# Kernel tuning notes

Hardware: AMD Instinct MI355X
Metric: run time of the kernel (lower is better)

Reference implementation:

```python
import jax, jax.numpy as jnp
import numpy as np

EMBED_DIM = 1024
HEAD = 16
DK = EMBED_DIM // HEAD  # 64
B, S = 2, 2048
NEG = -1.0e9


def setup_inputs() -> dict:
    key = jax.random.key(0)
    ks = jax.random.split(key, 8)
    d = {
        'query': jax.random.normal(ks[0], (B, S, EMBED_DIM), jnp.float32),
        'key': jax.random.normal(ks[1], (B, S, EMBED_DIM), jnp.float32),
        'value': jax.random.normal(ks[2], (B, S, EMBED_DIM), jnp.float32),
        'masked': jax.random.randint(ks[3], (B, S, S), 0, 2).astype(bool),
        'Wq': jax.random.normal(ks[4], (EMBED_DIM, EMBED_DIM), jnp.float32) / np.sqrt(EMBED_DIM),
        'Wk': jax.random.normal(ks[5], (EMBED_DIM, EMBED_DIM), jnp.float32) / np.sqrt(EMBED_DIM),
        'Wv': jax.random.normal(ks[6], (EMBED_DIM, EMBED_DIM), jnp.float32) / np.sqrt(EMBED_DIM),
        'Wo': jax.random.normal(ks[7], (EMBED_DIM, EMBED_DIM), jnp.float32) / np.sqrt(EMBED_DIM),
    }
    return d


def reference(query, key, value, masked, Wq, Wk, Wv, Wo):
    # projections (bias-free Linear: x @ W), split into heads: [B, H, S, DK]
    def split_heads(x):
        b, s, _ = x.shape
        return x.reshape(b, s, HEAD, DK).transpose(0, 2, 1, 3)

    q = split_heads(query @ Wq)
    k = split_heads(key @ Wk)
    v = split_heads(value @ Wv)

    scale = 1.0 / jnp.sqrt(jnp.asarray(DK, q.dtype))
    scores = jnp.einsum('bhqd,bhkd->bhqk', q, k) * scale
    scores = jnp.where(masked[:, None, :, :], NEG, scores)
    attn = jax.nn.softmax(scores, axis=-1)
    out = jnp.einsum('bhqk,bhkd->bhqd', attn, v)  # [B, H, S, DK]
    out = out.transpose(0, 2, 1, 3).reshape(query.shape[0], -1, EMBED_DIM)
    return out @ Wo
```

## Files before the change

### kernel.cpp

```cpp
#include <hip/hip_runtime.h>
#include <hip/hip_bf16.h>

typedef float f32x4 __attribute__((ext_vector_type(4)));
typedef __bf16 bf16x8 __attribute__((ext_vector_type(8)));
typedef _Float16 f16x2 __attribute__((ext_vector_type(2)));
typedef _Float16 f16x4 __attribute__((ext_vector_type(4)));

__device__ __forceinline__ unsigned short f2bf(float f){
  unsigned int u = __builtin_bit_cast(unsigned int, f);
  u += 0x7fffu + ((u >> 16) & 1u);
  return (unsigned short)(u >> 16);
}
__device__ __forceinline__ float bf2f(unsigned short h){
  return __builtin_bit_cast(float, (unsigned int)h << 16);
}

__device__ __forceinline__ f16x2 pkrtz(float a, float b){
  return __builtin_bit_cast(f16x2, __builtin_amdgcn_cvt_pkrtz(a, b));
}

__device__ __forceinline__ void glds16(const void* g, void* l){
  __builtin_amdgcn_global_load_lds((const __attribute__((address_space(1))) void*)g,
                                   (__attribute__((address_space(3))) void*)l, 16, 0, 0);
}

__device__ __forceinline__ f32x4 mfma16(bf16x8 a, bf16x8 b, f32x4 c){
  return __builtin_amdgcn_mfma_f32_16x16x32_bf16(a, b, c, 0, 0, 0);
}
__device__ __forceinline__ f32x4 mfma16h(f16x4 a, f16x4 b, f32x4 c){
  return __builtin_amdgcn_mfma_f32_16x16x16f16(a, b, c, 0, 0, 0);
}

#if __has_builtin(__builtin_amdgcn_exp2f)
__device__ __forceinline__ float exp2v(float x){ return __builtin_amdgcn_exp2f(x); }
#else
__device__ __forceinline__ float exp2v(float x){ return exp2f(x); }
#endif

__global__ void pack_mask_kernel(const unsigned char* __restrict__ m8,
                                 unsigned int* __restrict__ mp){
  const int wid = threadIdx.x >> 6, lane = threadIdx.x & 63;
  const int row = blockIdx.x * 4 + wid;
  const unsigned int* w32 = (const unsigned int*)m8;
  int bad = 0;
  #pragma unroll
  for(int c = 0; c < 1024; c += 64) bad |= (w32[c + lane] > 1u);
  const int is32 = !__any(bad);
  const int* m32 = (const int*)m8;
  for(int c0 = 0; c0 < 2048; c0 += 64){
    int mv = is32 ? m32[(size_t)row*2048 + c0 + lane]
                  : (int)m8[(size_t)row*2048 + c0 + lane];
    unsigned long long b = __ballot(mv != 0);
    if(lane == 0){
      mp[(size_t)row*64 + (c0 >> 5)]     = (unsigned int)b;
      mp[(size_t)row*64 + (c0 >> 5) + 1] = (unsigned int)(b >> 32);
    }
  }
}

__global__ void cvt3_kernel(const float* __restrict__ qs, const float* __restrict__ ks,
                            const float* __restrict__ vs, unsigned short* __restrict__ dst){
  const float* src = (blockIdx.y==0)?qs:(blockIdx.y==1)?ks:vs;
  unsigned short* d = dst + (size_t)blockIdx.y * 4194304;
  int i = blockIdx.x * 256 + threadIdx.x;
  const float4* s = (const float4*)src;
  float4 a = s[2*i], b = s[2*i+1];
  union { unsigned short h[8]; uint4 v; } o;
  o.h[0]=f2bf(a.x); o.h[1]=f2bf(a.y); o.h[2]=f2bf(a.z); o.h[3]=f2bf(a.w);
  o.h[4]=f2bf(b.x); o.h[5]=f2bf(b.y); o.h[6]=f2bf(b.z); o.h[7]=f2bf(b.w);
  ((uint4*)d)[i] = o.v;
}

__global__ void transW_kernel(const float* __restrict__ Wq, const float* __restrict__ Wk,
                              const float* __restrict__ Wv, const float* __restrict__ Wo,
                              unsigned short* __restrict__ WT){
  const float* W = (blockIdx.y==0)?Wq:(blockIdx.y==1)?Wk:(blockIdx.y==2)?Wv:Wo;
  const float scale = (blockIdx.y==0) ? 0.1803368801111601f : 1.0f;
  unsigned short* D = WT + (size_t)blockIdx.y * 1048576;
  int r0 = (blockIdx.x >> 4) * 64, c0 = (blockIdx.x & 15) * 64;
  __shared__ unsigned short T[64][65];
  int t = threadIdx.x;
  {
    int r = t >> 2, cb = (t & 3) * 16;
    const float4* src = (const float4*)(W + (size_t)(r0 + r) * 1024 + (c0 + cb));
    float4 v0 = src[0], v1 = src[1], v2 = src[2], v3 = src[3];
    float vals[16] = {v0.x,v0.y,v0.z,v0.w, v1.x,v1.y,v1.z,v1.w,
                      v2.x,v2.y,v2.z,v2.w, v3.x,v3.y,v3.z,v3.w};
    #pragma unroll
    for(int j=0;j<16;j++) T[cb + j][r] = f2bf(vals[j] * scale);
  }
  __syncthreads();
  {
    int c = t >> 2, rb = (t & 3) * 16;
    union { unsigned short h[16]; uint4 v[2]; } o;
    #pragma unroll
    for(int j=0;j<16;j++) o.h[j] = T[c][rb + j];
    uint4* dp = (uint4*)(D + (size_t)(c0 + c) * 1024 + (r0 + rb));
    dp[0] = o.v[0]; dp[1] = o.v[1];
  }
}

template<int OUTF32>
__global__ __launch_bounds__(256,2) void gemm_bt(
    const unsigned short* __restrict__ A0, const unsigned short* __restrict__ A1, const unsigned short* __restrict__ A2,
    const unsigned short* __restrict__ B0, const unsigned short* __restrict__ B1, const unsigned short* __restrict__ B2,
    unsigned short* __restrict__ C0, unsigned short* __restrict__ C1, unsigned short* __restrict__ C2,
    float* __restrict__ Cf)
{
  const unsigned short* A  = (blockIdx.z==0)?A0:(blockIdx.z==1)?A1:A2;
  const unsigned short* BT = (blockIdx.z==0)?B0:(blockIdx.z==1)?B1:B2;
  unsigned short* C        = (blockIdx.z==0)?C0:(blockIdx.z==1)?C1:C2;
  __shared__ unsigned short Asm[2][128*64];
  __shared__ unsigned short Bsm[2][128*64];
  const int wid = threadIdx.x >> 6, lane = threadIdx.x & 63;
  const int m0 = blockIdx.x * 128, n0 = blockIdx.y * 128;
  const int wrow = wid >> 1, wcol = wid & 1;
  const int li = lane & 15, lg = lane >> 4, li7 = lane & 7;
  f32x4 acc[4][4] = {};
  const int sr = lane >> 3;
  const int sc = lane & 7;
  const int sblk = sc ^ sr;

  #pragma unroll
  for(int i=0;i<4;i++){
    int r = wid*32 + i*8 + sr;
    glds16(A  + (size_t)(m0 + r)*1024 + sblk*8, &Asm[0][(wid*32 + i*8)*64]);
    glds16(BT + (size_t)(n0 + r)*1024 + sblk*8, &Bsm[0][(wid*32 + i*8)*64]);
  }
  __syncthreads();

  int buf = 0;
  for(int kt = 0; kt < 16; ++kt){
    if(kt < 15){
      const int kofs = (kt + 1) * 64;
      #pragma unroll
      for(int i=0;i<4;i++){
        int r = wid*32 + i*8 + sr;
        glds16(A  + (size_t)(m0 + r)*1024 + kofs + sblk*8, &Asm[buf^1][(wid*32 + i*8)*64]);
        glds16(BT + (size_t)(n0 + r)*1024 + kofs + sblk*8, &Bsm[buf^1][(wid*32 + i*8)*64]);
      }
    }
    #pragma unroll
    for(int kk=0; kk<2; kk++){
      bf16x8 af[4], bfv[4];
      #pragma unroll
      for(int fm=0; fm<4; fm++){
        int row = wrow*64 + fm*16 + li;
        int blk = (kk*4 + lg) ^ li7;
        af[fm] = *(const bf16x8*)&Asm[buf][row*64 + blk*8];
      }
      #pragma unroll
      for(int fn=0; fn<4; fn++){
        int row = wcol*64 + fn*16 + li;
        int blk = (kk*4 + lg) ^ li7;
        bfv[fn] = *(const bf16x8*)&Bsm[buf][row*64 + blk*8];
      }
      __builtin_amdgcn_s_setprio(1);
      #pragma unroll
      for(int fm=0; fm<4; fm++)
        #pragma unroll
        for(int fn=0; fn<4; fn++)
          acc[fm][fn] = mfma16(af[fm], bfv[fn], acc[fm][fn]);
      __builtin_amdgcn_s_setprio(0);
    }
    __syncthreads();
    buf ^= 1;
  }
  if(OUTF32 == 0 && blockIdx.z == 2){
    #pragma unroll
    for(int fm=0; fm<4; fm++){
      #pragma unroll
      for(int fn=0; fn<4; fn++){
        int col  = n0 + wcol*64 + fn*16 + li;
        int rowb = m0 + wrow*64 + fm*16 + lg*4;
        int bq = rowb >> 11, s = rowb & 2047;
        union { f16x2 h2[2]; unsigned long long u; } o;
        o.h2[0] = pkrtz(acc[fm][fn][0], acc[fm][fn][1]);
        o.h2[1] = pkrtz(acc[fm][fn][2], acc[fm][fn][3]);
        *(unsigned long long*)&C[((size_t)(bq*16 + (col>>6))*64 + (col&63))*2048 + s] = o.u;
      }
    }
  } else {
    #pragma unroll
    for(int fm=0; fm<4; fm++){
      #pragma unroll
      for(int fn=0; fn<4; fn++){
        int col  = n0 + wcol*64 + fn*16 + li;
        int rowb = m0 + wrow*64 + fm*16 + lg*4;
        #pragma unroll
        for(int r=0;r<4;r++){
          if(OUTF32) Cf[(size_t)(rowb + r)*1024 + col] = acc[fm][fn][r];
          else       C [(size_t)(rowb + r)*1024 + col] = f2bf(acc[fm][fn][r]);
        }
      }
    }
  }
}

__global__ __launch_bounds__(256,2) void attn_kernel(
    const unsigned short* __restrict__ Q, const unsigned short* __restrict__ K,
    const unsigned short* __restrict__ Vt, unsigned short* __restrict__ O,
    const unsigned int* __restrict__ mp)
{
  __shared__ unsigned short Ksm[2][64*64];
  __shared__ unsigned short Vsm[2][64*64];
  const int wid = threadIdx.x >> 6, lane = threadIdx.x & 63;
  const int orig = blockIdx.x;
  const int wg = (orig & 7) * 64 + (orig >> 3);
  const int qt = wg & 15, bh = wg >> 4;
  const int b = bh >> 4, h = bh & 15;
  const int q0 = qt * 128;
  const int li = lane & 15, lg = lane >> 4;
  const int li7 = li & 7;

  const int rowA = b*2048 + q0 + wid*32 + li;
  const int rowB = rowA + 16;

  bf16x8 qfA[2], qfB[2];
  {
    const unsigned short* qa = Q + (size_t)rowA*1024 + h*64 + lg*8;
    const unsigned short* qb = Q + (size_t)rowB*1024 + h*64 + lg*8;
    qfA[0] = *(const bf16x8*)qa; qfA[1] = *(const bf16x8*)(qa + 32);
    qfB[0] = *(const bf16x8*)qb; qfB[1] = *(const bf16x8*)(qb + 32);
  }

  f32x4 oaccA[4] = {}, oaccB[4] = {};
  float lrowA = 0.f, lrowB = 0.f;

  const int srow = lane >> 3;
  const int sblk = (lane & 7) ^ srow;

  #pragma unroll
  for(int i=0;i<2;i++){
    int r = wid*16 + i*8 + srow;
    glds16(K  + (size_t)(b*2048 + r)*1024 + h*64 + sblk*8, &Ksm[0][(wid*16 + i*8)*64]);
    glds16(Vt + (size_t)(bh*64 + r)*2048 + sblk*8,         &Vsm[0][(wid*16 + i*8)*64]);
  }
  uint2 mwA = *(const uint2*)&mp[(size_t)rowA*64];
  uint2 mwB = *(const uint2*)&mp[(size_t)rowB*64];
  uint2 mwAn, mwBn;
  __syncthreads();

  int buf = 0;
  for(int t = 0; t < 32; ++t){
    const int kv0 = t * 64;
    if(t < 31){
      #pragma unroll
      for(int i=0;i<2;i++){
        int r = wid*16 + i*8 + srow;
        glds16(K  + (size_t)(b*2048 + kv0 + 64 + r)*1024 + h*64 + sblk*8, &Ksm[buf^1][(wid*16 + i*8)*64]);
        glds16(Vt + (size_t)(bh*64 + r)*2048 + kv0 + 64 + sblk*8,         &Vsm[buf^1][(wid*16 + i*8)*64]);
      }
      mwAn = *(const uint2*)&mp[(size_t)rowA*64 + (size_t)((kv0 + 64) >> 5)];
      mwBn = *(const uint2*)&mp[(size_t)rowB*64 + (size_t)((kv0 + 64) >> 5)];
    }
    f32x4 pA[4], pB[4];
    __builtin_amdgcn_s_setprio(1);
    #pragma unroll
    for(int f=0; f<4; f++){
      f32x4 sa = {0.f,0.f,0.f,0.f}, sb = {0.f,0.f,0.f,0.f};
      #pragma unroll
      for(int kf=0; kf<2; kf++){
        int blk = (kf*4 + lg) ^ li7;
        bf16x8 kfr = *(const bf16x8*)&Ksm[buf][(f*16 + li)*64 + blk*8];
        sa = mfma16(kfr, qfA[kf], sa);
        sb = mfma16(kfr, qfB[kf], sb);
      }
      pA[f] = sa; pB[f] = sb;
    }
    __builtin_amdgcn_s_setprio(0);
    #pragma unroll
    for(int f=0; f<4; f++){
      unsigned int wA = (f < 2) ? mwA.x : mwA.y;
      unsigned int wB = (f < 2) ? mwB.x : mwB.y;
      float eA[4], eB[4];
      #pragma unroll
      for(int j=0;j<4;j++){
        unsigned int bitA = (wA >> ((f & 1)*16 + lg*4 + j)) & 1u;
        unsigned int bitB = (wB >> ((f & 1)*16 + lg*4 + j)) & 1u;
        float vA = exp2v(pA[f][j]);
        float vB = exp2v(pB[f][j]);
        eA[j] = bitA ? 0.f : vA;
        eB[j] = bitB ? 0.f : vB;
      }
      lrowA += (eA[0] + eA[1]) + (eA[2] + eA[3]);
      lrowB += (eB[0] + eB[1]) + (eB[2] + eB[3]);
      union { f16x2 h2[2]; f16x4 v; } ua, ub;
      ua.h2[0] = pkrtz(eA[0], eA[1]);
      ua.h2[1] = pkrtz(eA[2], eA[3]);
      ub.h2[0] = pkrtz(eB[0], eB[1]);
      ub.h2[1] = pkrtz(eB[2], eB[3]);
      const int blk = (f*2 + (lg >> 1)) ^ li7;
      const int sub = (lg & 1)*4;
      __builtin_amdgcn_s_setprio(1);
      #pragma unroll
      for(int dt=0; dt<4; dt++){
        f16x4 vf = *(const f16x4*)&Vsm[buf][(dt*16 + li)*64 + blk*8 + sub];
        oaccA[dt] = mfma16h(ua.v, vf, oaccA[dt]);
        oaccB[dt] = mfma16h(ub.v, vf, oaccB[dt]);
      }
      __builtin_amdgcn_s_setprio(0);
    }
    __syncthreads();
    mwA = mwAn; mwB = mwBn;
    buf ^= 1;
  }
  float rsA = lrowA, rsB = lrowB;
  rsA += __shfl_xor(rsA, 16); rsA += __shfl_xor(rsA, 32);
  rsB += __shfl_xor(rsB, 16); rsB += __shfl_xor(rsB, 32);
  float invA = 1.0f / rsA;
  float invB = 1.0f / rsB;
  #pragma unroll
  for(int r=0;r<4;r++){
    float ioA = __shfl(invA, lg*4 + r);
    float ioB = __shfl(invB, lg*4 + r);
    size_t rbA = (size_t)(b*2048 + q0 + wid*32 + lg*4 + r);
    size_t rbB = rbA + 16;
    #pragma unroll
    for(int dt=0; dt<4; dt++){
      O[rbA*1024 + h*64 + 16*dt + li] = f2bf(oaccA[dt][r] * ioA);
      O[rbB*1024 + h*64 + 16*dt + li] = f2bf(oaccB[dt][r] * ioB);
    }
  }
}

extern "C" void kernel_launch(void* const* d_in, const int* in_sizes, int n_in,
                              void* d_out, int out_size, void* d_ws, size_t ws_size,
                              hipStream_t stream)
{
  const float* q_in = (const float*)d_in[0];
  const float* k_in = (const float*)d_in[1];
  const float* v_in = (const float*)d_in[2];
  const unsigned char* mask = (const unsigned char*)d_in[3];
  const float* Wq = (const float*)d_in[4];
  const float* Wk = (const float*)d_in[5];
  const float* Wv = (const float*)d_in[6];
  const float* Wo = (const float*)d_in[7];

  char* ws = (char*)d_ws;
  const size_t MB = 1024*1024;
  unsigned short* XQ = (unsigned short*)(ws + 256);
  unsigned short* XK = (unsigned short*)(ws + 256 + 8*MB);
  unsigned short* XV = (unsigned short*)(ws + 256 + 16*MB);
  unsigned short* WT = (unsigned short*)(ws + 256 + 24*MB);
  unsigned short* Qb = (unsigned short*)(ws + 256 + 32*MB);
  unsigned short* Kb = (unsigned short*)(ws + 256 + 40*MB);
  unsigned short* Vt = (unsigned short*)(ws + 256 + 48*MB);
  unsigned short* Ob = XQ;
  unsigned int*   mpk= (unsigned int*)XV;

  cvt3_kernel<<<dim3(2048,3), 256, 0, stream>>>(q_in, k_in, v_in, XQ);
  transW_kernel<<<dim3(256,4), 256, 0, stream>>>(Wq, Wk, Wv, Wo, WT);
  gemm_bt<0><<<dim3(32,8,3), 256, 0, stream>>>(XQ, XK, XV,
                                               WT, WT + 1048576, WT + 2097152,
                                               Qb, Kb, Vt, nullptr);
  pack_mask_kernel<<<1024, 256, 0, stream>>>(mask, mpk);
  attn_kernel<<<512, 256, 0, stream>>>(Qb, Kb, Vt, Ob, mpk);
  gemm_bt<1><<<dim3(32,8,1), 256, 0, stream>>>(Ob, Ob, Ob,
                                               WT + 3*1048576, WT + 3*1048576, WT + 3*1048576,
                                               nullptr, nullptr, nullptr, (float*)d_out);
}
```

Measured before the change: 151.1 us.

## Double KV tile to 128 in attention and single-buffer projection GEMM

The attention kernel now stages 128 keys/values per iteration, with a 16-wide XOR swizzle for the V tile and 128-bit mask loads, which halves the number of loop iterations and barriers. The projection GEMM drops its double-buffered LDS prefetch in favour of a single buffer loaded and synced every k-step. That lowers LDS use but exposes global load latency, since loads no longer overlap compute. The larger attention tile raises LDS per block, which may limit occupancy.

Measured after the change: 145.5 us. 1.04x faster.

```diff
diff --git a/kernel.cpp b/kernel.cpp
--- a/kernel.cpp
+++ b/kernel.cpp
@@ -110,8 +110,8 @@
   const unsigned short* A  = (blockIdx.z==0)?A0:(blockIdx.z==1)?A1:A2;
   const unsigned short* BT = (blockIdx.z==0)?B0:(blockIdx.z==1)?B1:B2;
   unsigned short* C        = (blockIdx.z==0)?C0:(blockIdx.z==1)?C1:C2;
-  __shared__ unsigned short Asm[2][128*64];
-  __shared__ unsigned short Bsm[2][128*64];
+  __shared__ unsigned short Asm[128*64];
+  __shared__ unsigned short Bsm[128*64];
   const int wid = threadIdx.x >> 6, lane = threadIdx.x & 63;
   const int m0 = blockIdx.x * 128, n0 = blockIdx.y * 128;
   const int wrow = wid >> 1, wcol = wid & 1;
@@ -119,27 +119,17 @@
   f32x4 acc[4][4] = {};
   const int sr = lane >> 3;
   const int sc = lane & 7;
-  const int sblk = sc ^ sr;
-
-  #pragma unroll
-  for(int i=0;i<4;i++){
-    int r = wid*32 + i*8 + sr;
-    glds16(A  + (size_t)(m0 + r)*1024 + sblk*8, &Asm[0][(wid*32 + i*8)*64]);
-    glds16(BT + (size_t)(n0 + r)*1024 + sblk*8, &Bsm[0][(wid*32 + i*8)*64]);
-  }
-  __syncthreads();
-
-  int buf = 0;
+
   for(int kt = 0; kt < 16; ++kt){
-    if(kt < 15){
-      const int kofs = (kt + 1) * 64;
-      #pragma unroll
-      for(int i=0;i<4;i++){
-        int r = wid*32 + i*8 + sr;
-        glds16(A  + (size_t)(m0 + r)*1024 + kofs + sblk*8, &Asm[buf^1][(wid*32 + i*8)*64]);
-        glds16(BT + (size_t)(n0 + r)*1024 + kofs + sblk*8, &Bsm[buf^1][(wid*32 + i*8)*64]);
-      }
-    }
+    const int kofs = kt * 64;
+    #pragma unroll
+    for(int i=0;i<4;i++){
+      int r = wid*32 + i*8 + sr;
+      int blk = sc ^ sr;
+      glds16(A  + (size_t)(m0 + r)*1024 + kofs + blk*8, &Asm[(wid*32 + i*8)*64]);
+      glds16(BT + (size_t)(n0 + r)*1024 + kofs + blk*8, &Bsm[(wid*32 + i*8)*64]);
+    }
+    __syncthreads();
     #pragma unroll
     for(int kk=0; kk<2; kk++){
       bf16x8 af[4], bfv[4];
@@ -147,13 +137,13 @@
       for(int fm=0; fm<4; fm++){
         int row = wrow*64 + fm*16 + li;
         int blk = (kk*4 + lg) ^ li7;
-        af[fm] = *(const bf16x8*)&Asm[buf][row*64 + blk*8];
+        af[fm] = *(const bf16x8*)&Asm[row*64 + blk*8];
       }
       #pragma unroll
       for(int fn=0; fn<4; fn++){
         int row = wcol*64 + fn*16 + li;
         int blk = (kk*4 + lg) ^ li7;
-        bfv[fn] = *(const bf16x8*)&Bsm[buf][row*64 + blk*8];
+        bfv[fn] = *(const bf16x8*)&Bsm[row*64 + blk*8];
       }
       __builtin_amdgcn_s_setprio(1);
       #pragma unroll
@@ -164,7 +154,6 @@
       __builtin_amdgcn_s_setprio(0);
     }
     __syncthreads();
-    buf ^= 1;
   }
   if(OUTF32 == 0 && blockIdx.z == 2){
     #pragma unroll
@@ -202,8 +191,8 @@
     const unsigned short* __restrict__ Vt, unsigned short* __restrict__ O,
     const unsigned int* __restrict__ mp)
 {
-  __shared__ unsigned short Ksm[2][64*64];
-  __shared__ unsigned short Vsm[2][64*64];
+  __shared__ unsigned short Ksm[2][128*64];
+  __shared__ unsigned short Vsm[2][64*128];
   const int wid = threadIdx.x >> 6, lane = threadIdx.x & 63;
   const int orig = blockIdx.x;
   const int wg = (orig & 7) * 64 + (orig >> 3);
@@ -227,79 +216,96 @@
   f32x4 oaccA[4] = {}, oaccB[4] = {};
   float lrowA = 0.f, lrowB = 0.f;
 
-  const int srow = lane >> 3;
-  const int sblk = (lane & 7) ^ srow;
+  const int kr  = lane >> 3;
+  const int kblk = (lane & 7) ^ kr;
+  const int vr  = lane >> 4;
+  const int vc  = lane & 15;
 
   #pragma unroll
-  for(int i=0;i<2;i++){
-    int r = wid*16 + i*8 + srow;
-    glds16(K  + (size_t)(b*2048 + r)*1024 + h*64 + sblk*8, &Ksm[0][(wid*16 + i*8)*64]);
-    glds16(Vt + (size_t)(bh*64 + r)*2048 + sblk*8,         &Vsm[0][(wid*16 + i*8)*64]);
-  }
-  uint2 mwA = *(const uint2*)&mp[(size_t)rowA*64];
-  uint2 mwB = *(const uint2*)&mp[(size_t)rowB*64];
-  uint2 mwAn, mwBn;
+  for(int i=0;i<4;i++){
+    int krow = wid*32 + i*8 + kr;
+    glds16(K + (size_t)(b*2048 + krow)*1024 + h*64 + kblk*8, &Ksm[0][(wid*32 + i*8)*64]);
+  }
+  #pragma unroll
+  for(int i=0;i<4;i++){
+    int vrow = wid*16 + i*4 + vr;
+    int vb = vc ^ (vrow & 15);
+    glds16(Vt + (size_t)(bh*64 + vrow)*2048 + vb*8, &Vsm[0][(wid*16 + i*4)*128]);
+  }
+  uint4 mwA = *(const uint4*)&mp[(size_t)rowA*64];
+  uint4 mwB = *(const uint4*)&mp[(size_t)rowB*64];
+  uint4 mwAn, mwBn;
   __syncthreads();
 
   int buf = 0;
-  for(int t = 0; t < 32; ++t){
-    const int kv0 = t * 64;
-    if(t < 31){
-      #pragma unroll
-      for(int i=0;i<2;i++){
-        int r = wid*16 + i*8 + srow;
-        glds16(K  + (size_t)(b*2048 + kv0 + 64 + r)*1024 + h*64 + sblk*8, &Ksm[buf^1][(wid*16 + i*8)*64]);
-        glds16(Vt + (size_t)(bh*64 + r)*2048 + kv0 + 64 + sblk*8,         &Vsm[buf^1][(wid*16 + i*8)*64]);
-      }
-      mwAn = *(const uint2*)&mp[(size_t)rowA*64 + (size_t)((kv0 + 64) >> 5)];
-      mwBn = *(const uint2*)&mp[(size_t)rowB*64 + (size_t)((kv0 + 64) >> 5)];
-    }
-    f32x4 pA[4], pB[4];
-    __builtin_amdgcn_s_setprio(1);
-    #pragma unroll
-    for(int f=0; f<4; f++){
-      f32x4 sa = {0.f,0.f,0.f,0.f}, sb = {0.f,0.f,0.f,0.f};
-      #pragma unroll
-      for(int kf=0; kf<2; kf++){
-        int blk = (kf*4 + lg) ^ li7;
-        bf16x8 kfr = *(const bf16x8*)&Ksm[buf][(f*16 + li)*64 + blk*8];
-        sa = mfma16(kfr, qfA[kf], sa);
-        sb = mfma16(kfr, qfB[kf], sb);
-      }
-      pA[f] = sa; pB[f] = sb;
-    }
-    __builtin_amdgcn_s_setprio(0);
-    #pragma unroll
-    for(int f=0; f<4; f++){
-      unsigned int wA = (f < 2) ? mwA.x : mwA.y;
-      unsigned int wB = (f < 2) ? mwB.x : mwB.y;
-      float eA[4], eB[4];
-      #pragma unroll
-      for(int j=0;j<4;j++){
-        unsigned int bitA = (wA >> ((f & 1)*16 + lg*4 + j)) & 1u;
-        unsigned int bitB = (wB >> ((f & 1)*16 + lg*4 + j)) & 1u;
-        float vA = exp2v(pA[f][j]);
-        float vB = exp2v(pB[f][j]);
-        eA[j] = bitA ? 0.f : vA;
-        eB[j] = bitB ? 0.f : vB;
-      }
-      lrowA += (eA[0] + eA[1]) + (eA[2] + eA[3]);
-      lrowB += (eB[0] + eB[1]) + (eB[2] + eB[3]);
-      union { f16x2 h2[2]; f16x4 v; } ua, ub;
-      ua.h2[0] = pkrtz(eA[0], eA[1]);
-      ua.h2[1] = pkrtz(eA[2], eA[3]);
-      ub.h2[0] = pkrtz(eB[0], eB[1]);
-      ub.h2[1] = pkrtz(eB[2], eB[3]);
-      const int blk = (f*2 + (lg >> 1)) ^ li7;
-      const int sub = (lg & 1)*4;
+  for(int t = 0; t < 16; ++t){
+    if(t < 15){
+      const int kv = (t + 1) * 128;
+      #pragma unroll
+      for(int i=0;i<4;i++){
+        int krow = wid*32 + i*8 + kr;
+        glds16(K + (size_t)(b*2048 + kv + krow)*1024 + h*64 + kblk*8, &Ksm[buf^1][(wid*32 + i*8)*64]);
+      }
+      #pragma unroll
+      for(int i=0;i<4;i++){
+        int vrow = wid*16 + i*4 + vr;
+        int vb = vc ^ (vrow & 15);
+        glds16(Vt + (size_t)(bh*64 + vrow)*2048 + kv + vb*8, &Vsm[buf^1][(wid*16 + i*4)*128]);
+      }
+      mwAn = *(const uint4*)&mp[(size_t)rowA*64 + (size_t)(t + 1)*4];
+      mwBn = *(const uint4*)&mp[(size_t)rowB*64 + (size_t)(t + 1)*4];
+    }
+    #pragma unroll
+    for(int hlf = 0; hlf < 2; ++hlf){
+      f32x4 pA[4], pB[4];
       __builtin_amdgcn_s_setprio(1);
       #pragma unroll
-      for(int dt=0; dt<4; dt++){
-        f16x4 vf = *(const f16x4*)&Vsm[buf][(dt*16 + li)*64 + blk*8 + sub];
-        oaccA[dt] = mfma16h(ua.v, vf, oaccA[dt]);
-        oaccB[dt] = mfma16h(ub.v, vf, oaccB[dt]);
+      for(int f=0; f<4; f++){
+        f32x4 sa = {0.f,0.f,0.f,0.f}, sb = {0.f,0.f,0.f,0.f};
+        #pragma unroll
+        for(int kf=0; kf<2; kf++){
+          int blk = (kf*4 + lg) ^ li7;
+          bf16x8 kfr = *(const bf16x8*)&Ksm[buf][(hlf*64 + f*16 + li)*64 + blk*8];
+          sa = mfma16(kfr, qfA[kf], sa);
+          sb = mfma16(kfr, qfB[kf], sb);
+        }
+        pA[f] = sa; pB[f] = sb;
       }
       __builtin_amdgcn_s_setprio(0);
+      const unsigned int wA0 = hlf ? mwA.z : mwA.x, wA1 = hlf ? mwA.w : mwA.y;
+      const unsigned int wB0 = hlf ? mwB.z : mwB.x, wB1 = hlf ? mwB.w : mwB.y;
+      #pragma unroll
+      for(int f=0; f<4; f++){
+        unsigned int wA = (f < 2) ? wA0 : wA1;
+        unsigned int wB = (f < 2) ? wB0 : wB1;
+        float eA[4], eB[4];
+        #pragma unroll
+        for(int j=0;j<4;j++){
+          unsigned int bitA = (wA >> ((f & 1)*16 + lg*4 + j)) & 1u;
+          unsigned int bitB = (wB >> ((f & 1)*16 + lg*4 + j)) & 1u;
+          float vA = exp2v(pA[f][j]);
+          float vB = exp2v(pB[f][j]);
+          eA[j] = bitA ? 0.f : vA;
+          eB[j] = bitB ? 0.f : vB;
+        }
+        lrowA += (eA[0] + eA[1]) + (eA[2] + eA[3]);
+        lrowB += (eB[0] + eB[1]) + (eB[2] + eB[3]);
+        union { f16x2 h2[2]; f16x4 v; } ua, ub;
+        ua.h2[0] = pkrtz(eA[0], eA[1]);
+        ua.h2[1] = pkrtz(eA[2], eA[3]);
+        ub.h2[0] = pkrtz(eB[0], eB[1]);
+        ub.h2[1] = pkrtz(eB[2], eB[3]);
+        const int cb = (hlf*8 + f*2 + (lg >> 1)) ^ li;
+        const int sub = (lg & 1)*4;
+        __builtin_amdgcn_s_setprio(1);
+        #pragma unroll
+        for(int dt=0; dt<4; dt++){
+          f16x4 vf = *(const f16x4*)&Vsm[buf][(dt*16 + li)*128 + cb*8 + sub];
+          oaccA[dt] = mfma16h(ua.v, vf, oaccA[dt]);
+          oaccB[dt] = mfma16h(ub.v, vf, oaccB[dt]);
+        }
+        __builtin_amdgcn_s_setprio(0);
+      }
     }
     __syncthreads();
     mwA = mwAn; mwB = mwBn;
```
